# Optimization experiments

Measured on AMD Instinct MI355X. Metric: run time of the kernel, lower is better.

The kernel has to match this reference:

```python
import jax, jax.numpy as jnp
import numpy as np

DIM = 768
HEADS = 12
DIM_HEAD = 64
INNER = HEADS * DIM_HEAD  # 768
N = 197  # num_patches + 1
B = 64


def setup_inputs() -> dict:
    key = jax.random.key(0)
    k0, k1, k2, k3, k4 = jax.random.split(key, 5)
    x = jax.random.normal(k0, (B, N, DIM), dtype=jnp.float32)
    # Linear weights stored as [in, out] for x @ W
    W_qkv = jax.random.normal(k1, (DIM, 3 * INNER), dtype=jnp.float32) * (1.0 / np.sqrt(DIM))
    W_out = jax.random.normal(k2, (INNER, DIM), dtype=jnp.float32) * (1.0 / np.sqrt(INNER))
    b_out = jnp.zeros((DIM,), dtype=jnp.float32)
    scale = jnp.full((HEADS,), DIM_HEAD ** -0.5, dtype=jnp.float32)
    return {"x": x, "scale": scale, "W_qkv": W_qkv, "W_out": W_out, "b_out": b_out}


def reference(x, scale, W_qkv, W_out, b_out):
    b, n, _ = x.shape
    qkv = x @ W_qkv  # [b, n, 3*inner]
    q, k, v = jnp.split(qkv, 3, axis=-1)
    def to_heads(t):
        return t.reshape(b, n, HEADS, DIM_HEAD).transpose(0, 2, 1, 3)  # b h n d
    q, k, v = to_heads(q), to_heads(k), to_heads(v)
    # per-head learnable scale applied to raw dot products
    dots = jnp.einsum('bhid,bhjd->bhij', q, k) * scale[None, :, None, None]
    # diagonal self-mask: set dots[i,i] = -inf before softmax
    diag = jnp.eye(n, dtype=bool)[None, None]
    dots = jnp.where(diag, -jnp.inf, dots)
    attn = jax.nn.softmax(dots, axis=-1)
    out = jnp.einsum('bhij,bhjd->bhid', attn, v)
    out = out.transpose(0, 2, 1, 3).reshape(b, n, INNER)
    return out @ W_out + b_out
```

## Files before the change

kernel.cpp:

```cpp
#include <hip/hip_runtime.h>
#include <hip/hip_bf16.h>

typedef __attribute__((ext_vector_type(8))) short short8;
typedef __attribute__((ext_vector_type(4))) float floatx4;

#define MFMA_BF16(a, b, c) __builtin_amdgcn_mfma_f32_16x16x32_bf16((a), (b), (c), 0, 0, 0)

__device__ __forceinline__ unsigned short f2bf(float f) {
    union { float f; unsigned u; } v; v.f = f;
    unsigned r = v.u + 0x7fffu + ((v.u >> 16) & 1u);
    return (unsigned short)(r >> 16);
}

__device__ __forceinline__ void gload16(const unsigned short* g, unsigned short* l) {
    __builtin_amdgcn_global_load_lds(
        (const __attribute__((address_space(1))) unsigned int*)g,
        (__attribute__((address_space(3))) unsigned int*)l, 16, 0, 0);
}

__global__ void cast_f32_to_bf16(const float* __restrict__ src,
                                 unsigned short* __restrict__ dst, int n4) {
    int i = blockIdx.x * blockDim.x + threadIdx.x;
    int stride = gridDim.x * blockDim.x;
    for (; i < n4; i += stride) {
        float4 f = reinterpret_cast<const float4*>(src)[i];
        ushort4 o;
        o.x = f2bf(f.x); o.y = f2bf(f.y); o.z = f2bf(f.z); o.w = f2bf(f.w);
        reinterpret_cast<ushort4*>(dst)[i] = o;
    }
}

__global__ void transpose_cast(const float* __restrict__ src,
                               unsigned short* __restrict__ dst, int R, int C) {
    __shared__ float tile[32][33];
    int c0 = blockIdx.x * 32, r0 = blockIdx.y * 32;
    int tx = threadIdx.x, ty = threadIdx.y;
#pragma unroll
    for (int i = 0; i < 32; i += 8)
        tile[ty + i][tx] = src[(long)(r0 + ty + i) * C + (c0 + tx)];
    __syncthreads();
#pragma unroll
    for (int i = 0; i < 32; i += 8)
        dst[(long)(c0 + ty + i) * R + (r0 + tx)] = f2bf(tile[tx][ty + i]);
}

template <bool OUT_BF16>
__global__ __launch_bounds__(256, 4) void gemm_bt(
    const unsigned short* __restrict__ A,
    const unsigned short* __restrict__ B,
    void* __restrict__ Cout,
    const float* __restrict__ bias,
    int M, int N, int K) {
    __shared__ __align__(16) unsigned short Alds[128 * 32];
    __shared__ __align__(16) unsigned short Blds[128 * 32];

    int tid = threadIdx.x;
    int lane = tid & 63, wave = tid >> 6;
    int m0 = blockIdx.y * 128, n0 = blockIdx.x * 128;
    int wm = (wave >> 1) * 64, wn = (wave & 1) * 64;

    floatx4 acc[4][4];
#pragma unroll
    for (int mi = 0; mi < 4; mi++)
#pragma unroll
        for (int ni = 0; ni < 4; ni++) acc[mi][ni] = (floatx4){0.f, 0.f, 0.f, 0.f};

    int srow = tid >> 2;
    int scol = (tid & 3) * 8;
    int ar0 = m0 + srow;       if (ar0 >= M) ar0 = M - 1;
    int ar1 = m0 + 64 + srow;  if (ar1 >= M) ar1 = M - 1;
    const unsigned short* ap0 = A + (long)ar0 * K + scol;
    const unsigned short* ap1 = A + (long)ar1 * K + scol;
    const unsigned short* bp0 = B + (long)(n0 + srow) * K + scol;
    const unsigned short* bp1 = B + (long)(n0 + 64 + srow) * K + scol;
    unsigned short* la0 = &Alds[srow * 32 + scol];
    unsigned short* la1 = &Alds[(64 + srow) * 32 + scol];
    unsigned short* lb0 = &Blds[srow * 32 + scol];
    unsigned short* lb1 = &Blds[(64 + srow) * 32 + scol];

    for (int k0 = 0; k0 < K; k0 += 32) {
        __syncthreads();
        gload16(ap0 + k0, la0);
        gload16(ap1 + k0, la1);
        gload16(bp0 + k0, lb0);
        gload16(bp1 + k0, lb1);
        __syncthreads();

        short8 af[4], bfr[4];
#pragma unroll
        for (int mi = 0; mi < 4; mi++)
            af[mi] = *reinterpret_cast<const short8*>(
                &Alds[(wm + mi * 16 + (lane & 15)) * 32 + (lane >> 4) * 8]);
#pragma unroll
        for (int ni = 0; ni < 4; ni++)
            bfr[ni] = *reinterpret_cast<const short8*>(
                &Blds[(wn + ni * 16 + (lane & 15)) * 32 + (lane >> 4) * 8]);
#pragma unroll
        for (int mi = 0; mi < 4; mi++)
#pragma unroll
            for (int ni = 0; ni < 4; ni++)
                acc[mi][ni] = MFMA_BF16(af[mi], bfr[ni], acc[mi][ni]);
    }

    if (OUT_BF16) {
        unsigned short* C = (unsigned short*)Cout;
#pragma unroll
        for (int mi = 0; mi < 4; mi++)
#pragma unroll
            for (int rr = 0; rr < 4; rr++) {
                int row = m0 + wm + mi * 16 + (lane >> 4) * 4 + rr;
                if (row < M) {
                    long rbase = (long)row * N + n0 + wn + (lane & 15);
#pragma unroll
                    for (int ni = 0; ni < 4; ni++)
                        C[rbase + ni * 16] = f2bf(acc[mi][ni][rr]);
                }
            }
    } else {
        float* C = (float*)Cout;
        float bv[4];
#pragma unroll
        for (int ni = 0; ni < 4; ni++) bv[ni] = bias[n0 + wn + ni * 16 + (lane & 15)];
#pragma unroll
        for (int mi = 0; mi < 4; mi++)
#pragma unroll
            for (int rr = 0; rr < 4; rr++) {
                int row = m0 + wm + mi * 16 + (lane >> 4) * 4 + rr;
                if (row < M) {
                    long rbase = (long)row * N + n0 + wn + (lane & 15);
#pragma unroll
                    for (int ni = 0; ni < 4; ni++)
                        C[rbase + ni * 16] = acc[mi][ni][rr] + bv[ni];
                }
            }
    }
}

__global__ __launch_bounds__(448, 2) void attn_kernel(
    const unsigned short* __restrict__ qkv,
    const float* __restrict__ scale,
    unsigned short* __restrict__ out) {
    const int N = 197, D3 = 2304;
    int b = blockIdx.x / 12, h = blockIdx.x % 12;
    int tid = threadIdx.x, lane = tid & 63, wave = tid >> 6;

    __shared__ __align__(16) unsigned short Klds[224 * 64];
    __shared__ __align__(16) unsigned short Vlds[64 * 224];
    __shared__ __align__(16) unsigned short Plds[7 * 16 * 32];

    const unsigned short* base = qkv + (long)b * N * D3 + h * 64;

    for (int idx = tid; idx < 224 * 8; idx += 448) {
        int r = idx >> 3, s = idx & 7;
        short8 v = {0, 0, 0, 0, 0, 0, 0, 0};
        if (r < N) v = *reinterpret_cast<const short8*>(base + (long)r * D3 + 768 + s * 8);
        *reinterpret_cast<short8*>(&Klds[r * 64 + (s ^ (r & 7)) * 8]) = v;
    }
    for (int idx = tid; idx < 224 * 8; idx += 448) {
        int j = idx >> 3, sg = idx & 7;
        short8 v = {0, 0, 0, 0, 0, 0, 0, 0};
        if (j < N) v = *reinterpret_cast<const short8*>(base + (long)j * D3 + 1536 + sg * 8);
        int s = j >> 3;
#pragma unroll
        for (int e = 0; e < 8; e++) {
            int d = sg * 8 + e;
            Vlds[d * 224 + (s ^ (d & 3)) * 8 + (j & 7)] = (unsigned short)v[e];
        }
    }
    __syncthreads();

    float sc = scale[h];
    unsigned short* Pw = &Plds[wave * (16 * 32)];

    for (int rtb = 0; rtb < 2; rtb++) {
        int rt = wave + rtb * 7;
        int i0 = rt * 16;
        int qrow = i0 + (lane & 15); if (qrow > N - 1) qrow = N - 1;
        const unsigned short* qp = base + (long)qrow * D3;
        short8 qf[2];
#pragma unroll
        for (int kb = 0; kb < 2; kb++)
            qf[kb] = *reinterpret_cast<const short8*>(qp + kb * 32 + (lane >> 4) * 8);

        floatx4 sf[14];
#pragma unroll
        for (int jt = 0; jt < 14; jt++) sf[jt] = (floatx4){0.f, 0.f, 0.f, 0.f};
#pragma unroll
        for (int jt = 0; jt < 14; jt++) {
#pragma unroll
            for (int kb = 0; kb < 2; kb++) {
                int r = jt * 16 + (lane & 15);
                int slot = kb * 4 + (lane >> 4);
                short8 kf = *reinterpret_cast<const short8*>(
                    &Klds[r * 64 + (slot ^ (r & 7)) * 8]);
                sf[jt] = MFMA_BF16(qf[kb], kf, sf[jt]);
            }
        }

        int rowg[4];
        float mx[4], sm[4];
#pragma unroll
        for (int rr = 0; rr < 4; rr++) { rowg[rr] = i0 + (lane >> 4) * 4 + rr; mx[rr] = -1e30f; }
#pragma unroll
        for (int jt = 0; jt < 14; jt++) {
            int col = jt * 16 + (lane & 15);
#pragma unroll
            for (int rr = 0; rr < 4; rr++) {
                float v = sf[jt][rr] * sc;
                if (col >= N || col == rowg[rr]) v = -1e30f;
                sf[jt][rr] = v;
                mx[rr] = fmaxf(mx[rr], v);
            }
        }
#pragma unroll
        for (int rr = 0; rr < 4; rr++) {
#pragma unroll
            for (int m = 1; m <= 8; m <<= 1)
                mx[rr] = fmaxf(mx[rr], __shfl_xor(mx[rr], m, 64));
            sm[rr] = 0.f;
        }
#pragma unroll
        for (int jt = 0; jt < 14; jt++)
#pragma unroll
            for (int rr = 0; rr < 4; rr++) {
                float p = __expf(sf[jt][rr] - mx[rr]);
                sf[jt][rr] = p;
                sm[rr] += p;
            }
#pragma unroll
        for (int rr = 0; rr < 4; rr++)
#pragma unroll
            for (int m = 1; m <= 8; m <<= 1)
                sm[rr] += __shfl_xor(sm[rr], m, 64);

        floatx4 oacc[4];
#pragma unroll
        for (int dt = 0; dt < 4; dt++) oacc[dt] = (floatx4){0.f, 0.f, 0.f, 0.f};
#pragma unroll
        for (int c = 0; c < 7; c++) {
#pragma unroll
            for (int jh = 0; jh < 2; jh++) {
#pragma unroll
                for (int rr = 0; rr < 4; rr++) {
                    int row = (lane >> 4) * 4 + rr;
                    int jj = jh * 16 + (lane & 15);
                    Pw[row * 32 + ((jj >> 3) ^ (row & 3)) * 8 + (jj & 7)] =
                        f2bf(sf[c * 2 + jh][rr]);
                }
            }
            int prow = lane & 15;
            short8 pa = *reinterpret_cast<const short8*>(
                &Pw[prow * 32 + (((lane >> 4)) ^ (prow & 3)) * 8]);
#pragma unroll
            for (int dt = 0; dt < 4; dt++) {
                int d = dt * 16 + (lane & 15);
                int slot = c * 4 + (lane >> 4);
                short8 vf = *reinterpret_cast<const short8*>(
                    &Vlds[d * 224 + (slot ^ (d & 3)) * 8]);
                oacc[dt] = MFMA_BF16(pa, vf, oacc[dt]);
            }
        }

#pragma unroll
        for (int rr = 0; rr < 4; rr++) {
            int n = rowg[rr];
            if (n < N) {
                float r = 1.f / sm[rr];
                long o = ((long)b * N + n) * 768 + h * 64;
#pragma unroll
                for (int dt = 0; dt < 4; dt++)
                    out[o + dt * 16 + (lane & 15)] = f2bf(oacc[dt][rr] * r);
            }
        }
    }
}

extern "C" void kernel_launch(void* const* d_in, const int* in_sizes, int n_in,
                              void* d_out, int out_size, void* d_ws, size_t ws_size,
                              hipStream_t stream) {
    (void)in_sizes; (void)n_in; (void)out_size; (void)ws_size;
    const float* x     = (const float*)d_in[0];
    const float* scale = (const float*)d_in[1];
    const float* Wqkv  = (const float*)d_in[2];
    const float* Wout  = (const float*)d_in[3];
    const float* bout  = (const float*)d_in[4];
    float* out = (float*)d_out;

    const int M = 12608;
    char* ws = (char*)d_ws;
    unsigned short* x_bf   = (unsigned short*)(ws);
    unsigned short* wqkv_t = (unsigned short*)(ws + 19365888);
    unsigned short* wout_t = (unsigned short*)(ws + 22904832);
    unsigned short* qkv    = (unsigned short*)(ws + 24084480);
    unsigned short* ao     = (unsigned short*)(ws + 82182144);

    cast_f32_to_bf16<<<2048, 256, 0, stream>>>(x, x_bf, (M * 768) / 4);
    transpose_cast<<<dim3(2304 / 32, 768 / 32), dim3(32, 8), 0, stream>>>(Wqkv, wqkv_t, 768, 2304);
    transpose_cast<<<dim3(768 / 32, 768 / 32), dim3(32, 8), 0, stream>>>(Wout, wout_t, 768, 768);
    gemm_bt<true><<<dim3(2304 / 128, 99), 256, 0, stream>>>(x_bf, wqkv_t, qkv, nullptr, M, 2304, 768);
    attn_kernel<<<768, 448, 0, stream>>>(qkv, scale, ao);
    gemm_bt<false><<<dim3(768 / 128, 99), 256, 0, stream>>>(ao, wout_t, out, bout, M, 768, 768);
}
```

Measured before the change: 219.7 us.

## Deepen GEMM K-tile to 64 with XOR-swizzled LDS, trim attention key tiles

The GEMM now stages a 64-wide K slice per iteration into swizzled LDS, which halves the number of barrier-separated load rounds and uses an XOR swizzle to avoid LDS bank conflicts. The attention kernel computes scores over 13 key tiles of 16 (208 columns) instead of 14, which drops one fully padded tile of QK MFMAs and softmax work. The last P tile is filled with zeros. The larger LDS footprint per GEMM block could reduce occupancy.

```diff
diff --git a/kernel.cpp b/kernel.cpp
--- a/kernel.cpp
+++ b/kernel.cpp
@@ -51,8 +51,8 @@
     void* __restrict__ Cout,
     const float* __restrict__ bias,
     int M, int N, int K) {
-    __shared__ __align__(16) unsigned short Alds[128 * 32];
-    __shared__ __align__(16) unsigned short Blds[128 * 32];
+    __shared__ __align__(16) unsigned short Alds[128 * 64];
+    __shared__ __align__(16) unsigned short Blds[128 * 64];
 
     int tid = threadIdx.x;
     int lane = tid & 63, wave = tid >> 6;
@@ -65,41 +65,48 @@
 #pragma unroll
         for (int ni = 0; ni < 4; ni++) acc[mi][ni] = (floatx4){0.f, 0.f, 0.f, 0.f};
 
-    int srow = tid >> 2;
-    int scol = (tid & 3) * 8;
-    int ar0 = m0 + srow;       if (ar0 >= M) ar0 = M - 1;
-    int ar1 = m0 + 64 + srow;  if (ar1 >= M) ar1 = M - 1;
-    const unsigned short* ap0 = A + (long)ar0 * K + scol;
-    const unsigned short* ap1 = A + (long)ar1 * K + scol;
-    const unsigned short* bp0 = B + (long)(n0 + srow) * K + scol;
-    const unsigned short* bp1 = B + (long)(n0 + 64 + srow) * K + scol;
-    unsigned short* la0 = &Alds[srow * 32 + scol];
-    unsigned short* la1 = &Alds[(64 + srow) * 32 + scol];
-    unsigned short* lb0 = &Blds[srow * 32 + scol];
-    unsigned short* lb1 = &Blds[(64 + srow) * 32 + scol];
-
-    for (int k0 = 0; k0 < K; k0 += 32) {
+    int srow = tid >> 3;
+    int scol = (((tid & 7) ^ (srow & 7)) << 3);
+    const unsigned short* ap[4];
+    const unsigned short* bp[4];
+    unsigned short* la[4];
+    unsigned short* lb[4];
+#pragma unroll
+    for (int i = 0; i < 4; i++) {
+        int row = i * 32 + srow;
+        int ar = m0 + row; if (ar >= M) ar = M - 1;
+        ap[i] = A + (long)ar * K + scol;
+        bp[i] = B + (long)(n0 + row) * K + scol;
+        la[i] = &Alds[row * 64 + (tid & 7) * 8];
+        lb[i] = &Blds[row * 64 + (tid & 7) * 8];
+    }
+
+    for (int k0 = 0; k0 < K; k0 += 64) {
         __syncthreads();
-        gload16(ap0 + k0, la0);
-        gload16(ap1 + k0, la1);
-        gload16(bp0 + k0, lb0);
-        gload16(bp1 + k0, lb1);
+#pragma unroll
+        for (int i = 0; i < 4; i++) gload16(ap[i] + k0, la[i]);
+#pragma unroll
+        for (int i = 0; i < 4; i++) gload16(bp[i] + k0, lb[i]);
         __syncthreads();
 
-        short8 af[4], bfr[4];
-#pragma unroll
-        for (int mi = 0; mi < 4; mi++)
-            af[mi] = *reinterpret_cast<const short8*>(
-                &Alds[(wm + mi * 16 + (lane & 15)) * 32 + (lane >> 4) * 8]);
-#pragma unroll
-        for (int ni = 0; ni < 4; ni++)
-            bfr[ni] = *reinterpret_cast<const short8*>(
-                &Blds[(wn + ni * 16 + (lane & 15)) * 32 + (lane >> 4) * 8]);
-#pragma unroll
-        for (int mi = 0; mi < 4; mi++)
+#pragma unroll
+        for (int ks = 0; ks < 2; ks++) {
+            int sw = ((ks * 4 + (lane >> 4)) ^ (lane & 7)) * 8;
+            short8 af[4], bfr[4];
+#pragma unroll
+            for (int mi = 0; mi < 4; mi++)
+                af[mi] = *reinterpret_cast<const short8*>(
+                    &Alds[(wm + mi * 16 + (lane & 15)) * 64 + sw]);
 #pragma unroll
             for (int ni = 0; ni < 4; ni++)
-                acc[mi][ni] = MFMA_BF16(af[mi], bfr[ni], acc[mi][ni]);
+                bfr[ni] = *reinterpret_cast<const short8*>(
+                    &Blds[(wn + ni * 16 + (lane & 15)) * 64 + sw]);
+#pragma unroll
+            for (int mi = 0; mi < 4; mi++)
+#pragma unroll
+                for (int ni = 0; ni < 4; ni++)
+                    acc[mi][ni] = MFMA_BF16(af[mi], bfr[ni], acc[mi][ni]);
+        }
     }
 
     if (OUT_BF16) {
@@ -141,16 +148,17 @@
     const float* __restrict__ scale,
     unsigned short* __restrict__ out) {
     const int N = 197, D3 = 2304;
+    const int NT = 13;
     int b = blockIdx.x / 12, h = blockIdx.x % 12;
     int tid = threadIdx.x, lane = tid & 63, wave = tid >> 6;
 
-    __shared__ __align__(16) unsigned short Klds[224 * 64];
+    __shared__ __align__(16) unsigned short Klds[208 * 64];
     __shared__ __align__(16) unsigned short Vlds[64 * 224];
     __shared__ __align__(16) unsigned short Plds[7 * 16 * 32];
 
     const unsigned short* base = qkv + (long)b * N * D3 + h * 64;
 
-    for (int idx = tid; idx < 224 * 8; idx += 448) {
+    for (int idx = tid; idx < 208 * 8; idx += 448) {
         int r = idx >> 3, s = idx & 7;
         short8 v = {0, 0, 0, 0, 0, 0, 0, 0};
         if (r < N) v = *reinterpret_cast<const short8*>(base + (long)r * D3 + 768 + s * 8);
@@ -182,11 +190,11 @@
         for (int kb = 0; kb < 2; kb++)
             qf[kb] = *reinterpret_cast<const short8*>(qp + kb * 32 + (lane >> 4) * 8);
 
-        floatx4 sf[14];
-#pragma unroll
-        for (int jt = 0; jt < 14; jt++) sf[jt] = (floatx4){0.f, 0.f, 0.f, 0.f};
-#pragma unroll
-        for (int jt = 0; jt < 14; jt++) {
+        floatx4 sf[NT];
+#pragma unroll
+        for (int jt = 0; jt < NT; jt++) sf[jt] = (floatx4){0.f, 0.f, 0.f, 0.f};
+#pragma unroll
+        for (int jt = 0; jt < NT; jt++) {
 #pragma unroll
             for (int kb = 0; kb < 2; kb++) {
                 int r = jt * 16 + (lane & 15);
@@ -202,7 +210,7 @@
 #pragma unroll
         for (int rr = 0; rr < 4; rr++) { rowg[rr] = i0 + (lane >> 4) * 4 + rr; mx[rr] = -1e30f; }
 #pragma unroll
-        for (int jt = 0; jt < 14; jt++) {
+        for (int jt = 0; jt < NT; jt++) {
             int col = jt * 16 + (lane & 15);
 #pragma unroll
             for (int rr = 0; rr < 4; rr++) {
@@ -220,7 +228,7 @@
             sm[rr] = 0.f;
         }
 #pragma unroll
-        for (int jt = 0; jt < 14; jt++)
+        for (int jt = 0; jt < NT; jt++)
 #pragma unroll
             for (int rr = 0; rr < 4; rr++) {
                 float p = __expf(sf[jt][rr] - mx[rr]);
@@ -240,12 +248,13 @@
         for (int c = 0; c < 7; c++) {
 #pragma unroll
             for (int jh = 0; jh < 2; jh++) {
+                int jtc = c * 2 + jh;
 #pragma unroll
                 for (int rr = 0; rr < 4; rr++) {
                     int row = (lane >> 4) * 4 + rr;
                     int jj = jh * 16 + (lane & 15);
-                    Pw[row * 32 + ((jj >> 3) ^ (row & 3)) * 8 + (jj & 7)] =
-                        f2bf(sf[c * 2 + jh][rr]);
+                    float pv = (jtc < NT) ? sf[jtc < NT ? jtc : 0][rr] : 0.f;
+                    Pw[row * 32 + ((jj >> 3) ^ (row & 3)) * 8 + (jj & 7)] = f2bf(pv);
                 }
             }
             int prow = lane & 15;
```

Measured after the change: 204.7 us. -6.9%, faster.
